# Optimization experiments

Hardware: AMD Instinct MI355X
Metric: run time of the kernel (lower is better)

The kernel has to match this reference:

```python
import jax, jax.numpy as jnp
import numpy as np

KERNEL_MUL = 2.0
KERNEL_NUM = 5
STRUCT_W = 0.1

N_NODES = 4096
D_FEAT = 128
N_EDGES = 65536


def setup_inputs() -> dict:
    key = jax.random.key(0)
    k1, k2, k3, k4 = jax.random.split(key, 4)
    return {
        "source_features": jax.random.normal(k1, (N_NODES, D_FEAT), jnp.float32),
        "target_features": jax.random.normal(k2, (N_NODES, D_FEAT), jnp.float32),
        "source_edge_index": jax.random.randint(k3, (2, N_EDGES), 0, N_NODES, jnp.int32),
        "target_edge_index": jax.random.randint(k4, (2, N_EDGES), 0, N_NODES, jnp.int32),
    }


def _augment(feats, edge_index):
    # feats: [n, d]; edge_index: [2, E]
    n = feats.shape[0]
    # in-degree (torch_geometric degree on edge_index[1]), normalized by n-1
    deg = jnp.zeros(n, feats.dtype).at[edge_index[1]].add(1.0)
    norm_deg = deg / (n - 1)
    # dense adjacency (to_dense_adj sums duplicate edges)
    A = jnp.zeros((n, n), feats.dtype).at[edge_index[0], edge_index[1]].add(1.0)
    M = (A > 0).astype(feats.dtype)  # binary neighbor mask (nonzero rows)
    d = M.sum(axis=1)  # number of neighbors per node
    # triangles[v] = sum_{i,j in N(v)} A[i,j] / 2  == ((M @ A) * M).sum(1) / 2
    tri = ((M @ A) * M).sum(axis=1) / 2.0
    max_edges = d * (d - 1) / 2.0
    clustering = jnp.where(d >= 2.0, tri / jnp.maximum(max_edges, 1.0), 0.0)
    struct = jnp.stack([norm_deg, jnp.log1p(clustering)], axis=1)  # [n, 2]
    return jnp.concatenate([feats, STRUCT_W * struct], axis=1)


def _rbf_mmd(X, Y):
    nx, ny = X.shape[0], Y.shape[0]
    XY = jnp.concatenate([X, Y], axis=0)  # [N, d+2]
    sq = jnp.sum(XY * XY, axis=1)
    # squared euclidean distances (cdist ** 2), clamped for numerical safety
    dists = jnp.maximum(sq[:, None] + sq[None, :] - 2.0 * (XY @ XY.T), 0.0)
    N = nx + ny
    # adaptive bandwidth: median of strictly-upper-triangle distances
    triu_mask = jnp.triu(jnp.ones((N, N), bool), k=1)
    sigma = jnp.nanmedian(jnp.where(triu_mask, dists, jnp.nan))
    K = jnp.zeros_like(dists)
    for i in range(KERNEL_NUM):  # fixed small multiscale loop
        bw = sigma * (KERNEL_MUL ** (i - KERNEL_NUM // 2))
        K = K + jnp.exp(-dists / (2.0 * bw))
    K = K / KERNEL_NUM
    K_XX, K_YY, K_XY = K[:nx, :nx], K[nx:, nx:], K[:nx, nx:]
    mxx = (K_XX.sum() - jnp.trace(K_XX)) / (nx * (nx - 1))
    myy = (K_YY.sum() - jnp.trace(K_YY)) / (ny * (ny - 1))
    mxy = K_XY.mean()
    return jnp.maximum(mxx + myy - 2.0 * mxy, 0.0)


def reference(source_features, target_features, source_edge_index, target_edge_index):
    X = _augment(source_features, source_edge_index)
    Y = _augment(target_features, target_edge_index)
    return _rbf_mmd(X, Y)
```

## Files before the change

### kernel.cpp

```cpp
#include <hip/hip_runtime.h>
#include <math.h>

#define NN    4096
#define DF    128
#define NE    65536
#define NTOT  8192
#define TILE  128
#define KC    44
#define NTILE 64
#define NBLK  2080
#define R0    16775167u
#define R1    16775168u
#define FINF  __int_as_float(0x7f800000)

#define OFF_MB   0ULL
#define OFF_H1   4194304ULL
#define OFF_HMID 4210688ULL
#define OFF_HLOW 4218880ULL
#define OFF_DEG  4227072ULL
#define OFF_TRI  4259840ULL
#define ZERO_BYTES 4292608ULL
#define OFF_XYT  4292608ULL
#define OFF_SQ   8617984ULL
#define OFF_BS   8650752ULL
#define OFF_SEL  8667392ULL
#define OFF_SIG  8667456ULL
#define OFF_D    8667520ULL
#define DBYTES   136314880ULL
#define WS_CACHED (OFF_D + DBYTES)


__global__ __launch_bounds__(256) void build_k(const int* __restrict__ eiS, const int* __restrict__ eiT,
                                               unsigned* __restrict__ Mb, int* __restrict__ degc){
  int gid = blockIdx.x*256 + threadIdx.x;
  int g = gid >> 16, e = gid & 65535;
  const int* ei = g ? eiT : eiS;
  unsigned* M = Mb + (size_t)g*NN*128;
  int* dg = degc + g*NN;
  int s = ei[e], t = ei[NE + e];
  atomicOr(&M[(size_t)s*128 + (t>>5)], 1u << (t&31));
  atomicAdd(&dg[t], 1);
}

#define GPB 16
__global__ __launch_bounds__(256) void tri_k(const int* __restrict__ eiS, const int* __restrict__ eiT,
                                             const unsigned* __restrict__ Mb, int* __restrict__ tric){
  int g  = blockIdx.x >> 8;
  int nb = blockIdx.x & 255;
  const int* ei = g ? eiT : eiS;
  const unsigned* M = Mb + (size_t)g*NN*128;
  int* tr = tric + g*NN;
  __shared__ unsigned lm[128*20];
  __shared__ int lcnt[GPB];
  int tid = threadIdx.x;
  for(int idx=tid; idx<128*GPB; idx+=256){
    int w = idx & 127, gg = idx >> 7;
    lm[w*20+gg] = M[(size_t)(nb*GPB+gg)*128 + w];
  }
  if(tid < GPB) lcnt[tid]=0;
  __syncthreads();
  int cnt[GPB];
  #pragma unroll
  for(int q=0;q<GPB;++q) cnt[q]=0;
  for(int e=tid; e<NE; e+=256){
    int s = ei[e], t = ei[NE+e];
    int ws_ = s>>5, bs = s&31, wt = t>>5, bt = t&31;
    const uint4* ps4 = (const uint4*)&lm[ws_*20];
    const uint4* pt4 = (const uint4*)&lm[wt*20];
    unsigned a_[GPB], b_[GPB];
    ((uint4*)a_)[0]=ps4[0]; ((uint4*)a_)[1]=ps4[1]; ((uint4*)a_)[2]=ps4[2]; ((uint4*)a_)[3]=ps4[3];
    ((uint4*)b_)[0]=pt4[0]; ((uint4*)b_)[1]=pt4[1]; ((uint4*)b_)[2]=pt4[2]; ((uint4*)b_)[3]=pt4[3];
    #pragma unroll
    for(int q=0;q<GPB;++q) cnt[q] += (int)((a_[q]>>bs) & (b_[q]>>bt) & 1u);
  }
  #pragma unroll
  for(int q=0;q<GPB;++q){
    int v = cnt[q];
    for(int off=32; off; off>>=1) v += __shfl_down(v, off);
    if((tid&63)==0) atomicAdd(&lcnt[q], v);
  }
  __syncthreads();
  if(tid < GPB) tr[nb*GPB + tid] = lcnt[tid];
}

__global__ __launch_bounds__(64) void finalize_k(const float* __restrict__ featS, const float* __restrict__ featT,
                                                 const unsigned* __restrict__ Mb, const int* __restrict__ degc,
                                                 const int* __restrict__ tric, float* __restrict__ XYT,
                                                 float* __restrict__ sq){
  int b = blockIdx.x;
  int g = b >> 12, i = b & 4095;
  int lane = threadIdx.x;
  const unsigned* Mr = Mb + (size_t)g*NN*128 + (size_t)i*128;
  int pc = __popc(Mr[lane]) + __popc(Mr[64+lane]);
  for(int off=32; off; off>>=1) pc += __shfl_down(pc, off);
  pc = __shfl(pc, 0);
  const float* feats = g ? featT : featS;
  int n = g*NN + i;
  float v0 = feats[(size_t)i*DF + lane];
  float v1 = feats[(size_t)i*DF + 64 + lane];
  XYT[(size_t)lane*NTOT + n]      = v0;
  XYT[(size_t)(64+lane)*NTOT + n] = v1;
  float s0 = v0*v0 + v1*v1;
  if(lane==0){
    float degf = (float)degc[g*NN+i];
    float nd   = degf / 4095.0f;
    float dd   = (float)pc;
    float tri  = 0.5f * (float)tric[g*NN+i];
    float me   = dd*(dd-1.0f)*0.5f;
    float cl   = (dd >= 2.0f) ? (tri / fmaxf(me, 1.0f)) : 0.0f;
    float f0 = 0.1f * nd;
    float f1 = 0.1f * log1pf(cl);
    XYT[(size_t)128*NTOT + n] = f0;
    XYT[(size_t)129*NTOT + n] = f1;
    XYT[(size_t)130*NTOT + n] = 0.0f;
    XYT[(size_t)131*NTOT + n] = 0.0f;
    s0 += f0*f0 + f1*f1;
  }
  for(int off=32; off; off>>=1) s0 += __shfl_down(s0, off);
  if(lane==0) sq[g*NN+i] = s0;
}

template<int MODE>
__global__ __launch_bounds__(256) void pair_k(const float* __restrict__ XYT, const float* __restrict__ sq,
                                              unsigned* __restrict__ hist1, unsigned* __restrict__ hmid,
                                              unsigned* __restrict__ hlow, const unsigned* __restrict__ sel,
                                              const float* __restrict__ sigp, double* __restrict__ blockSums,
                                              float* __restrict__ Dout){
  int t = blockIdx.x, bi = 0;
  while(t >= NTILE - bi){ t -= NTILE - bi; ++bi; }
  int bj = bi + t;
  __shared__ float4 smem4[2816];
  float* As = (float*)smem4;
  float* Bs = As + KC*TILE;
  int tid = threadIdx.x;
  int trw = tid >> 4, tcl = tid & 15;
  float acc[8][8];
  #pragma unroll
  for(int r=0;r<8;++r){
    #pragma unroll
    for(int c=0;c<8;++c) acc[r][c]=0.f;
  }
  int i0 = bi*TILE, j0 = bj*TILE;
  for(int kc=0; kc<3; ++kc){
    #pragma unroll
    for(int s=0;s<11;++s){
      int idx = tid + s*256;
      int isB = idx >= 1408;
      int l = isB ? (idx-1408) : idx;
      int k = l >> 5, c4 = l & 31;
      int col = (isB ? j0 : i0) + c4*4;
      smem4[idx] = *(const float4*)&XYT[(size_t)(kc*KC+k)*NTOT + col];
    }
    __syncthreads();
    #pragma unroll 4
    for(int k=0;k<KC;++k){
      float a[8], b[8];
      const float* Ak = As + k*TILE;
      const float* Bk = Bs + k*TILE;
      *(float4*)&a[0] = *(const float4*)&Ak[trw*8];
      *(float4*)&a[4] = *(const float4*)&Ak[trw*8+4];
      *(float4*)&b[0] = *(const float4*)&Bk[tcl*8];
      *(float4*)&b[4] = *(const float4*)&Bk[tcl*8+4];
      #pragma unroll
      for(int r=0;r<8;++r){
        #pragma unroll
        for(int c=0;c<8;++c) acc[r][c] = fmaf(a[r], b[c], acc[r][c]);
      }
    }
    __syncthreads();
  }
  float sqi[8], sqj[8];
  #pragma unroll
  for(int r=0;r<8;++r) sqi[r] = sq[i0 + trw*8 + r];
  #pragma unroll
  for(int c=0;c<8;++c) sqj[c] = sq[j0 + tcl*8 + c];

  if constexpr (MODE==0 || MODE==3){
    unsigned* lh = (unsigned*)smem4;
    for(int x=tid;x<4096;x+=256) lh[x]=0u;
    __syncthreads();
    #pragma unroll
    for(int r=0;r<8;++r){
      float rowd[8];
      #pragma unroll
      for(int c=0;c<8;++c){
        int i = i0 + trw*8 + r, j = j0 + tcl*8 + c;
        bool valid = (bi!=bj) || (i<j);
        float d = fmaxf(sqi[r]+sqj[c]-2.0f*acc[r][c], 0.0f);
        rowd[c] = valid ? d : FINF;
        if(valid) atomicAdd(&lh[__float_as_uint(d)>>20], 1u);
      }
      if constexpr (MODE==3){
        float* rp = Dout + (size_t)blockIdx.x*16384 + (size_t)(trw*8+r)*128 + tcl*8;
        *(float4*)rp       = make_float4(rowd[0],rowd[1],rowd[2],rowd[3]);
        *(float4*)(rp+4)   = make_float4(rowd[4],rowd[5],rowd[6],rowd[7]);
      }
    }
    __syncthreads();
    for(int x=tid;x<4096;x+=256){ unsigned v=lh[x]; if(v) atomicAdd(&hist1[x], v); }
  } else if constexpr (MODE==4 || MODE==5){
    unsigned* lh2 = (unsigned*)smem4;
    for(int x=tid;x<2048;x+=256) lh2[x]=0u;
    __syncthreads();
    unsigned m0, m1;
    if constexpr (MODE==4){ m0=sel[0]; m1=sel[1]; }
    else                  { m0=(sel[0]<<10)|sel[4]; m1=(sel[1]<<10)|sel[5]; }
    #pragma unroll
    for(int r=0;r<8;++r){
      #pragma unroll
      for(int c=0;c<8;++c){
        int i = i0 + trw*8 + r, j = j0 + tcl*8 + c;
        if(bi!=bj || i<j){
          float d = fmaxf(sqi[r]+sqj[c]-2.0f*acc[r][c], 0.0f);
          unsigned bits = __float_as_uint(d);
          unsigned key = (MODE==4) ? (bits>>20) : (bits>>10);
          unsigned bin = (MODE==4) ? ((bits>>10)&1023u) : (bits&1023u);
          if(key==m0)      atomicAdd(&lh2[bin], 1u);
          else if(key==m1) atomicAdd(&lh2[1024+bin], 1u);
        }
      }
    }
    __syncthreads();
    unsigned* hout = (MODE==4) ? hmid : hlow;
    for(int x=tid;x<2048;x+=256){ unsigned v=lh2[x]; if(v) atomicAdd(&hout[x], v); }
  } else {
    float sig = *sigp;
    float inv = 1.0f/sig;
    float k0=2.0f*inv, k1=inv, k2=0.5f*inv, k3=0.25f*inv, k4=0.125f*inv;
    double lsum = 0.0;
    #pragma unroll
    for(int r=0;r<8;++r){
      #pragma unroll
      for(int c=0;c<8;++c){
        int i = i0 + trw*8 + r, j = j0 + tcl*8 + c;
        if(bi!=bj || i<j){
          float d = fmaxf(sqi[r]+sqj[c]-2.0f*acc[r][c], 0.0f);
          float kv = expf(-d*k0)+expf(-d*k1)+expf(-d*k2)+expf(-d*k3)+expf(-d*k4);
          lsum += (double)kv;
        }
      }
    }
    for(int off=32; off; off>>=1) lsum += __shfl_down(lsum, off);
    double* redbuf = (double*)smem4;
    if((tid&63)==0) redbuf[tid>>6] = lsum;
    __syncthreads();
    if(tid==0) blockSums[blockIdx.x] = (redbuf[0]+redbuf[1]+redbuf[2]+redbuf[3])*0.2;
  }
}

template<int LVL>
__global__ __launch_bounds__(256) void hist_stream_k(const float* __restrict__ D, const unsigned* __restrict__ sel,
                                                     unsigned* __restrict__ hout){
  __shared__ unsigned lh[2048];
  int tid = threadIdx.x;
  for(int x=tid;x<2048;x+=256) lh[x]=0u;
  __syncthreads();
  unsigned m0, m1;
  if constexpr (LVL==0){ m0=sel[0]; m1=sel[1]; }
  else                 { m0=(sel[0]<<10)|sel[4]; m1=(sel[1]<<10)|sel[5]; }
  const float4* P = (const float4*)(D + (size_t)blockIdx.x*16384);
  #pragma unroll
  for(int k=0;k<16;++k){
    float4 v = P[tid + k*256];
    float vals[4] = {v.x, v.y, v.z, v.w};
    #pragma unroll
    for(int q=0;q<4;++q){
      unsigned bits = __float_as_uint(vals[q]);
      unsigned key = (LVL==0) ? (bits>>20) : (bits>>10);
      unsigned bin = (LVL==0) ? ((bits>>10)&1023u) : (bits&1023u);
      if(key==m0)      atomicAdd(&lh[bin], 1u);
      else if(key==m1) atomicAdd(&lh[1024+bin], 1u);
    }
  }
  __syncthreads();
  for(int x=tid;x<2048;x+=256){ unsigned v=lh[x]; if(v) atomicAdd(&hout[x], v); }
}

__global__ __launch_bounds__(256) void ksum_k(const float* __restrict__ D, const float* __restrict__ sigp,
                                              double* __restrict__ blockSums){
  float sig = *sigp;
  float inv = 1.0f/sig;
  float k0=2.0f*inv, k1=inv, k2=0.5f*inv, k3=0.25f*inv, k4=0.125f*inv;
  const float4* P = (const float4*)(D + (size_t)blockIdx.x*16384);
  int tid = threadIdx.x;
  double lsum = 0.0;
  #pragma unroll
  for(int k=0;k<16;++k){
    float4 v = P[tid + k*256];
    float vals[4] = {v.x, v.y, v.z, v.w};
    #pragma unroll
    for(int q=0;q<4;++q){
      float d = vals[q];
      float kv = expf(-d*k0)+expf(-d*k1)+expf(-d*k2)+expf(-d*k3)+expf(-d*k4);
      lsum += (double)kv;
    }
  }
  for(int off=32; off; off>>=1) lsum += __shfl_down(lsum, off);
  __shared__ double redbuf[4];
  if((tid&63)==0) redbuf[tid>>6] = lsum;
  __syncthreads();
  if(tid==0) blockSums[blockIdx.x] = (redbuf[0]+redbuf[1]+redbuf[2]+redbuf[3])*0.2;
}

__global__ __launch_bounds__(256) void sel1_k(const unsigned* __restrict__ hist1, unsigned* __restrict__ sel){
  __shared__ unsigned part[256];
  int tid = threadIdx.x;
  unsigned s = 0;
  #pragma unroll
  for(int k=0;k<16;++k) s += hist1[tid*16+k];
  part[tid] = s;
  __syncthreads();
  if(tid==0){
    const unsigned ranks[2] = {R0, R1};
    unsigned segs[2], bases[2];
    unsigned cum = 0; int found = 0;
    for(int i=0; i<256 && found<2; ++i){
      unsigned nx = cum + part[i];
      while(found<2 && ranks[found] < nx){ segs[found]=i; bases[found]=cum; ++found; }
      cum = nx;
    }
    for(int tg=0; tg<2; ++tg){
      unsigned c2 = bases[tg];
      for(int b=segs[tg]*16;; ++b){
        unsigned nx = c2 + hist1[b];
        if(ranks[tg] < nx){ sel[tg]=(unsigned)b; sel[2+tg]=ranks[tg]-c2; break; }
        c2 = nx;
      }
    }
  }
}

__global__ __launch_bounds__(1024) void selB_k(const unsigned* __restrict__ hmid, unsigned* __restrict__ sel){
  __shared__ unsigned buf[1024];
  __shared__ unsigned res[4];
  int tid = threadIdx.x;
  for(int tgt=0; tgt<2; ++tgt){
    bool useA = (tgt==0) || (sel[1]==sel[0]);
    const unsigned* H = hmid + (useA ? 0 : 1024);
    unsigned rank = sel[2+tgt];
    buf[tid] = H[tid];
    __syncthreads();
    for(int off=1; off<1024; off<<=1){
      unsigned v = buf[tid];
      unsigned a = (tid>=off) ? buf[tid-off] : 0u;
      __syncthreads();
      buf[tid] = v + a;
      __syncthreads();
    }
    unsigned prev = tid ? buf[tid-1] : 0u;
    if(rank < buf[tid] && rank >= prev){ res[2*tgt]=(unsigned)tid; res[2*tgt+1]=rank-prev; }
    __syncthreads();
  }
  if(tid==0){ sel[4]=res[0]; sel[6]=res[1]; sel[5]=res[2]; sel[7]=res[3]; }
}

__global__ __launch_bounds__(1024) void selC_k(const unsigned* __restrict__ hlow, const unsigned* __restrict__ sel,
                                               float* __restrict__ sigp){
  __shared__ unsigned buf[1024];
  __shared__ unsigned outbits[2];
  int tid = threadIdx.x;
  for(int tgt=0; tgt<2; ++tgt){
    bool useA = (tgt==0) || ((sel[1]==sel[0]) && (sel[5]==sel[4]));
    const unsigned* H = hlow + (useA ? 0 : 1024);
    unsigned rank = sel[6+tgt];
    buf[tid] = H[tid];
    __syncthreads();
    for(int off=1; off<1024; off<<=1){
      unsigned v = buf[tid];
      unsigned a = (tid>=off) ? buf[tid-off] : 0u;
      __syncthreads();
      buf[tid] = v + a;
      __syncthreads();
    }
    unsigned prev = tid ? buf[tid-1] : 0u;
    if(rank < buf[tid] && rank >= prev){
      outbits[tgt] = (sel[tgt]<<20) | (sel[4+tgt]<<10) | (unsigned)tid;
    }
    __syncthreads();
  }
  if(tid==0){
    float v0 = __uint_as_float(outbits[0]);
    float v1 = __uint_as_float(outbits[1]);
    *sigp = 0.5f*(v0+v1);
  }
}

__global__ __launch_bounds__(256) void final_k(const double* __restrict__ blockSums, float* __restrict__ out){
  __shared__ double cls[3][256];
  int tid = threadIdx.x;
  double l0=0, l1=0, l2=0;
  for(int b=tid; b<NBLK; b+=256){
    int t=b, bi=0;
    while(t >= NTILE - bi){ t -= NTILE - bi; ++bi; }
    int bj = bi + t;
    double v = blockSums[b];
    if(bj < 32) l0 += v;
    else if(bi >= 32) l2 += v;
    else l1 += v;
  }
  cls[0][tid]=l0; cls[1][tid]=l1; cls[2][tid]=l2;
  __syncthreads();
  for(int off=128; off; off>>=1){
    if(tid<off){ cls[0][tid]+=cls[0][tid+off]; cls[1][tid]+=cls[1][tid+off]; cls[2][tid]+=cls[2][tid+off]; }
    __syncthreads();
  }
  if(tid==0){
    double sxx=cls[0][0], sxy=cls[1][0], syy=cls[2][0];
    double mxx = (2.0*sxx)/((double)NN*(NN-1));
    double myy = (2.0*syy)/((double)NN*(NN-1));
    double mxy = sxy/((double)NN*(double)NN);
    double r = mxx + myy - 2.0*mxy;
    out[0] = fmaxf((float)r, 0.0f);
  }
}

extern "C" void kernel_launch(void* const* d_in, const int* in_sizes, int n_in,
                              void* d_out, int out_size, void* d_ws, size_t ws_size,
                              hipStream_t stream){
  (void)in_sizes; (void)n_in; (void)out_size;
  const float* featS = (const float*)d_in[0];
  const float* featT = (const float*)d_in[1];
  const int*   eiS   = (const int*)d_in[2];
  const int*   eiT   = (const int*)d_in[3];
  char* ws = (char*)d_ws;
  unsigned* Mb    = (unsigned*)(ws + OFF_MB);
  unsigned* hist1 = (unsigned*)(ws + OFF_H1);
  unsigned* hmid  = (unsigned*)(ws + OFF_HMID);
  unsigned* hlow  = (unsigned*)(ws + OFF_HLOW);
  int*      degc  = (int*)(ws + OFF_DEG);
  int*      tric  = (int*)(ws + OFF_TRI);
  float*    XYT   = (float*)(ws + OFF_XYT);
  float*    sq    = (float*)(ws + OFF_SQ);
  double*   bsums = (double*)(ws + OFF_BS);
  unsigned* sel   = (unsigned*)(ws + OFF_SEL);
  float*    sigp  = (float*)(ws + OFF_SIG);
  float*    Dbuf  = (float*)(ws + OFF_D);
  float*    out   = (float*)d_out;

  const bool cached = (ws_size >= WS_CACHED);

  hipMemsetAsync(ws, 0, (size_t)ZERO_BYTES, stream);

  build_k   <<<512, 256, 0, stream>>>(eiS, eiT, Mb, degc);
  tri_k     <<<512, 256, 0, stream>>>(eiS, eiT, Mb, tric);
  finalize_k<<<NTOT, 64, 0, stream>>>(featS, featT, Mb, degc, tric, XYT, sq);

  if(cached){
    pair_k<3>       <<<NBLK, 256, 0, stream>>>(XYT, sq, hist1, hmid, hlow, sel, sigp, bsums, Dbuf);
    sel1_k          <<<1, 256, 0, stream>>>(hist1, sel);
    hist_stream_k<0><<<NBLK, 256, 0, stream>>>(Dbuf, sel, hmid);
    selB_k          <<<1, 1024, 0, stream>>>(hmid, sel);
    hist_stream_k<1><<<NBLK, 256, 0, stream>>>(Dbuf, sel, hlow);
    selC_k          <<<1, 1024, 0, stream>>>(hlow, sel, sigp);
    ksum_k          <<<NBLK, 256, 0, stream>>>(Dbuf, sigp, bsums);
  } else {
    pair_k<0>       <<<NBLK, 256, 0, stream>>>(XYT, sq, hist1, hmid, hlow, sel, sigp, bsums, Dbuf);
    sel1_k          <<<1, 256, 0, stream>>>(hist1, sel);
    pair_k<4>       <<<NBLK, 256, 0, stream>>>(XYT, sq, hist1, hmid, hlow, sel, sigp, bsums, Dbuf);
    selB_k          <<<1, 1024, 0, stream>>>(hmid, sel);
    pair_k<5>       <<<NBLK, 256, 0, stream>>>(XYT, sq, hist1, hmid, hlow, sel, sigp, bsums, Dbuf);
    selC_k          <<<1, 1024, 0, stream>>>(hlow, sel, sigp);
    pair_k<2>       <<<NBLK, 256, 0, stream>>>(XYT, sq, hist1, hmid, hlow, sel, sigp, bsums, Dbuf);
  }

  final_k  <<<1, 256, 0, stream>>>(bsums, out);
}
```

Measured before the change: 541.1 us.

## Transpose neighbor bitmasks per node in triangle kernel and stagger GEMM column reads

The triangle-count kernel now handles 32 nodes per block with 512 threads. It first builds a per-vertex 32-bit membership mask in shared memory, so each edge costs two shared loads plus one AND and a popcount-style accumulation, instead of loading sixteen words and shifting. The edge list is also re-read by half as many blocks. Separately, the pairwise GEMM tile now assigns each thread columns tcl*4 and 64+tcl*4 instead of eight contiguous columns, which is intended to cut LDS bank conflicts on the B operand; the sq lookups, index math and D output writes are updated to match.

```diff
diff --git a/kernel.cpp b/kernel.cpp
--- a/kernel.cpp
+++ b/kernel.cpp
@@ -42,45 +42,48 @@
   atomicAdd(&dg[t], 1);
 }
 
-#define GPB 16
-__global__ __launch_bounds__(256) void tri_k(const int* __restrict__ eiS, const int* __restrict__ eiT,
+#define GPB2 32
+__global__ __launch_bounds__(512) void tri_k(const int* __restrict__ eiS, const int* __restrict__ eiT,
                                              const unsigned* __restrict__ Mb, int* __restrict__ tric){
-  int g  = blockIdx.x >> 8;
-  int nb = blockIdx.x & 255;
+  int g  = blockIdx.x >> 7;
+  int nb = blockIdx.x & 127;
   const int* ei = g ? eiT : eiS;
   const unsigned* M = Mb + (size_t)g*NN*128;
-  int* tr = tric + g*NN;
-  __shared__ unsigned lm[128*20];
-  __shared__ int lcnt[GPB];
-  int tid = threadIdx.x;
-  for(int idx=tid; idx<128*GPB; idx+=256){
-    int w = idx & 127, gg = idx >> 7;
-    lm[w*20+gg] = M[(size_t)(nb*GPB+gg)*128 + w];
-  }
-  if(tid < GPB) lcnt[tid]=0;
-  __syncthreads();
-  int cnt[GPB];
-  #pragma unroll
-  for(int q=0;q<GPB;++q) cnt[q]=0;
-  for(int e=tid; e<NE; e+=256){
+  __shared__ unsigned rows[GPB2*128];
+  __shared__ unsigned mask[NN];
+  __shared__ int lcnt[GPB2];
+  int tid = threadIdx.x;
+  for(int idx=tid; idx<GPB2*128; idx+=512){
+    int q = idx >> 7, w = idx & 127;
+    rows[q*128 + w] = M[(size_t)(nb*GPB2+q)*128 + w];
+  }
+  if(tid < GPB2) lcnt[tid] = 0;
+  __syncthreads();
+  for(int j=tid; j<NN; j+=512){
+    int w = j >> 5, b = j & 31;
+    unsigned m = 0;
+    #pragma unroll
+    for(int q=0;q<GPB2;++q) m |= ((rows[q*128+w] >> b) & 1u) << q;
+    mask[j] = m;
+  }
+  __syncthreads();
+  int cnt[GPB2];
+  #pragma unroll
+  for(int q=0;q<GPB2;++q) cnt[q]=0;
+  for(int e=tid; e<NE; e+=512){
     int s = ei[e], t = ei[NE+e];
-    int ws_ = s>>5, bs = s&31, wt = t>>5, bt = t&31;
-    const uint4* ps4 = (const uint4*)&lm[ws_*20];
-    const uint4* pt4 = (const uint4*)&lm[wt*20];
-    unsigned a_[GPB], b_[GPB];
-    ((uint4*)a_)[0]=ps4[0]; ((uint4*)a_)[1]=ps4[1]; ((uint4*)a_)[2]=ps4[2]; ((uint4*)a_)[3]=ps4[3];
-    ((uint4*)b_)[0]=pt4[0]; ((uint4*)b_)[1]=pt4[1]; ((uint4*)b_)[2]=pt4[2]; ((uint4*)b_)[3]=pt4[3];
-    #pragma unroll
-    for(int q=0;q<GPB;++q) cnt[q] += (int)((a_[q]>>bs) & (b_[q]>>bt) & 1u);
-  }
-  #pragma unroll
-  for(int q=0;q<GPB;++q){
+    unsigned both = mask[s] & mask[t];
+    #pragma unroll
+    for(int q=0;q<GPB2;++q) cnt[q] += (int)((both>>q)&1u);
+  }
+  #pragma unroll
+  for(int q=0;q<GPB2;++q){
     int v = cnt[q];
     for(int off=32; off; off>>=1) v += __shfl_down(v, off);
     if((tid&63)==0) atomicAdd(&lcnt[q], v);
   }
   __syncthreads();
-  if(tid < GPB) tr[nb*GPB + tid] = lcnt[tid];
+  if(tid < GPB2) tric[g*NN + nb*GPB2 + tid] = lcnt[tid];
 }
 
 __global__ __launch_bounds__(64) void finalize_k(const float* __restrict__ featS, const float* __restrict__ featT,
@@ -159,8 +162,8 @@
       const float* Bk = Bs + k*TILE;
       *(float4*)&a[0] = *(const float4*)&Ak[trw*8];
       *(float4*)&a[4] = *(const float4*)&Ak[trw*8+4];
-      *(float4*)&b[0] = *(const float4*)&Bk[tcl*8];
-      *(float4*)&b[4] = *(const float4*)&Bk[tcl*8+4];
+      *(float4*)&b[0] = *(const float4*)&Bk[tcl*4];
+      *(float4*)&b[4] = *(const float4*)&Bk[64 + tcl*4];
       #pragma unroll
       for(int r=0;r<8;++r){
         #pragma unroll
@@ -173,7 +176,10 @@
   #pragma unroll
   for(int r=0;r<8;++r) sqi[r] = sq[i0 + trw*8 + r];
   #pragma unroll
-  for(int c=0;c<8;++c) sqj[c] = sq[j0 + tcl*8 + c];
+  for(int c=0;c<8;++c){
+    int col = (c<4) ? (tcl*4 + c) : (64 + tcl*4 + (c-4));
+    sqj[c] = sq[j0 + col];
+  }
 
   if constexpr (MODE==0 || MODE==3){
     unsigned* lh = (unsigned*)smem4;
@@ -184,16 +190,17 @@
       float rowd[8];
       #pragma unroll
       for(int c=0;c<8;++c){
-        int i = i0 + trw*8 + r, j = j0 + tcl*8 + c;
+        int col = (c<4) ? (tcl*4 + c) : (64 + tcl*4 + (c-4));
+        int i = i0 + trw*8 + r, j = j0 + col;
         bool valid = (bi!=bj) || (i<j);
         float d = fmaxf(sqi[r]+sqj[c]-2.0f*acc[r][c], 0.0f);
         rowd[c] = valid ? d : FINF;
         if(valid) atomicAdd(&lh[__float_as_uint(d)>>20], 1u);
       }
       if constexpr (MODE==3){
-        float* rp = Dout + (size_t)blockIdx.x*16384 + (size_t)(trw*8+r)*128 + tcl*8;
-        *(float4*)rp       = make_float4(rowd[0],rowd[1],rowd[2],rowd[3]);
-        *(float4*)(rp+4)   = make_float4(rowd[4],rowd[5],rowd[6],rowd[7]);
+        float* rp = Dout + (size_t)blockIdx.x*16384 + (size_t)(trw*8+r)*128;
+        *(float4*)(rp + tcl*4)      = make_float4(rowd[0],rowd[1],rowd[2],rowd[3]);
+        *(float4*)(rp + 64 + tcl*4) = make_float4(rowd[4],rowd[5],rowd[6],rowd[7]);
       }
     }
     __syncthreads();
@@ -209,7 +216,8 @@
     for(int r=0;r<8;++r){
       #pragma unroll
       for(int c=0;c<8;++c){
-        int i = i0 + trw*8 + r, j = j0 + tcl*8 + c;
+        int col = (c<4) ? (tcl*4 + c) : (64 + tcl*4 + (c-4));
+        int i = i0 + trw*8 + r, j = j0 + col;
         if(bi!=bj || i<j){
           float d = fmaxf(sqi[r]+sqj[c]-2.0f*acc[r][c], 0.0f);
           unsigned bits = __float_as_uint(d);
@@ -232,7 +240,8 @@
     for(int r=0;r<8;++r){
       #pragma unroll
       for(int c=0;c<8;++c){
-        int i = i0 + trw*8 + r, j = j0 + tcl*8 + c;
+        int col = (c<4) ? (tcl*4 + c) : (64 + tcl*4 + (c-4));
+        int i = i0 + trw*8 + r, j = j0 + col;
         if(bi!=bj || i<j){
           float d = fmaxf(sqi[r]+sqj[c]-2.0f*acc[r][c], 0.0f);
           float kv = expf(-d*k0)+expf(-d*k1)+expf(-d*k2)+expf(-d*k3)+expf(-d*k4);
@@ -442,7 +451,7 @@
   hipMemsetAsync(ws, 0, (size_t)ZERO_BYTES, stream);
 
   build_k   <<<512, 256, 0, stream>>>(eiS, eiT, Mb, degc);
-  tri_k     <<<512, 256, 0, stream>>>(eiS, eiT, Mb, tric);
+  tri_k     <<<256, 512, 0, stream>>>(eiS, eiT, Mb, tric);
   finalize_k<<<NTOT, 64, 0, stream>>>(featS, featT, Mb, degc, tric, XYT, sq);
 
   if(cached){
```

After: 481.8 us. -11.0%, faster.
